# Performance work log

Measured on AMD Instinct MI355X. Metric: run time of the kernel, lower is better.

Reference implementation:

```python
import jax, jax.numpy as jnp
import numpy as np

B, H, W, C, NH = 4, 64, 64, 512, 16
HD = C // NH
BIAS_LEVEL = 0.1
LN_EPS = 1e-5


def layernorm(x, g, b):
    m = jnp.mean(x, axis=-1, keepdims=True)
    v = jnp.mean(jnp.square(x - m), axis=-1, keepdims=True)
    return (x - m) * jax.lax.rsqrt(v + LN_EPS) * g + b


def partition(x, idx):
    # x: [B, L, C] -> windows [nW, S, C]
    xg = x.reshape(B, H, W, C)
    if idx == 0:  # horizontal strips: window = one row of length W
        return xg.reshape(B * H, W, C)
    else:  # vertical strips: window = one column of length H, ordered by column
        return xg.transpose(0, 2, 1, 3).reshape(B * W, H, C)


def unpartition(w, idx):
    # w: [nW, S, C] -> [B, L, C]
    if idx == 0:
        return w.reshape(B, H * W, C)
    else:
        return w.reshape(B, W, H, C).transpose(0, 2, 1, 3).reshape(B, H * W, C)


def eg_attention(q, k, v, res_x, rpe, idx):
    # q,k,v: [B, L, C]; res_x: [B, L, C]; rpe: [1, NH, S, S]
    S = rpe.shape[-1]
    nW = (B * H * W) // S

    def to_heads(t):
        return partition(t, idx).reshape(nW, S, NH, HD).transpose(0, 2, 1, 3)

    qh, kh, vh = to_heads(q), to_heads(k), to_heads(v)  # [nW, NH, S, HD]
    attn = jnp.einsum('whsd,whtd->whst', qh, kh) + BIAS_LEVEL * rpe
    # gating mask from raw scores
    M = jnp.mean(jnp.abs(attn), axis=(1, 2, 3), keepdims=True)  # [nW,1,1,1]
    M = M / jnp.max(M)
    M = jnp.maximum(M, 0.5)
    # L2-normalize rows, trig transform
    norm = jnp.sqrt(jnp.sum(jnp.square(attn), axis=-1, keepdims=True))
    attn = attn / jnp.maximum(norm, 1e-12)
    attn = 1.0 - jnp.cos(attn * (jnp.pi / 2))
    attn = attn * M
    out = jnp.einsum('whst,whtd->whsd', attn, vh)  # [nW, NH, S, HD]
    out = out.transpose(0, 2, 1, 3).reshape(nW, S, C)
    out = unpartition(out, idx)  # [B, L, C]
    # masked residual: res_x is chunked sequentially (row-major), as in the source
    res = res_x.reshape(nW, S, C) * (1.0 - M[:, 0])
    res = res.reshape(B, H * W, C)
    return out + res


def eg_block(x, rpe, idx, ln1_g, ln1_b, wqkv, wproj, bproj, ln2_g, ln2_b,
             wfc1, bfc1, wfc2, bfc2):
    img = layernorm(x, ln1_g, ln1_b)
    qkv = img @ wqkv  # [B, L, 3C]
    q, k, v = jnp.split(qkv, 3, axis=-1)
    att = eg_attention(q, k, v, x, rpe, idx)
    att = att @ wproj + bproj
    x = x + att
    h = layernorm(x, ln2_g, ln2_b)
    h = jax.nn.gelu(h @ wfc1 + bfc1, approximate=False) @ wfc2 + bfc2
    return x + h


def setup_inputs() -> dict:
    key = jax.random.key(0)
    ks = jax.random.split(key, 16)
    d = {
        'x': jax.random.normal(ks[0], (B, H * W, C), jnp.float32),
        'rpe0': jax.random.normal(ks[1], (1, NH, W, W), jnp.float32),
        'rpe1': jax.random.normal(ks[2], (1, NH, H, H), jnp.float32),
    }
    for i, blk in enumerate(['0', '1']):
        kk = jax.random.split(ks[3 + i], 8)
        d['ln1_g' + blk] = jnp.ones((C,), jnp.float32)
        d['ln1_b' + blk] = jnp.zeros((C,), jnp.float32)
        d['wqkv' + blk] = jax.random.normal(kk[0], (C, 3 * C), jnp.float32) * 0.02
        d['wproj' + blk] = jax.random.normal(kk[1], (C, C), jnp.float32) * 0.02
        d['bproj' + blk] = jnp.zeros((C,), jnp.float32)
        d['ln2_g' + blk] = jnp.ones((C,), jnp.float32)
        d['ln2_b' + blk] = jnp.zeros((C,), jnp.float32)
        d['wfc1_' + blk] = jax.random.normal(kk[2], (C, 4 * C), jnp.float32) * 0.02
        d['bfc1_' + blk] = jnp.zeros((4 * C,), jnp.float32)
        d['wfc2_' + blk] = jax.random.normal(kk[3], (4 * C, C), jnp.float32) * 0.02
        d['bfc2_' + blk] = jnp.zeros((C,), jnp.float32)
    return d


def reference(x, rpe0, rpe1,
              ln1_g0, ln1_b0, wqkv0, wproj0, bproj0, ln2_g0, ln2_b0,
              wfc1_0, bfc1_0, wfc2_0, bfc2_0,
              ln1_g1, ln1_b1, wqkv1, wproj1, bproj1, ln2_g1, ln2_b1,
              wfc1_1, bfc1_1, wfc2_1, bfc2_1):
    x = eg_block(x, rpe0, 0, ln1_g0, ln1_b0, wqkv0, wproj0, bproj0,
                 ln2_g0, ln2_b0, wfc1_0, bfc1_0, wfc2_0, bfc2_0)
    x = eg_block(x, rpe1, 1, ln1_g1, ln1_b1, wqkv1, wproj1, bproj1,
                 ln2_g1, ln2_b1, wfc1_1, bfc1_1, wfc2_1, bfc2_1)
    return x
```

## Files before the change

### kernel.cpp

```cpp
#include <hip/hip_runtime.h>
#include <cstdint>
#include <cstddef>

typedef __bf16 bf16;
typedef __attribute__((ext_vector_type(4))) float f32x4;
typedef __attribute__((ext_vector_type(8))) __bf16 bf16x8;
typedef __attribute__((ext_vector_type(4))) __bf16 bf16x4;

static __device__ __forceinline__ f32x4 mfma16(bf16x8 a, bf16x8 b, f32x4 c) {
    return __builtin_amdgcn_mfma_f32_16x16x32_bf16(a, b, c, 0, 0, 0);
}

#define GLOAD_LDS16(gsrc, ldst)                                              \
    __builtin_amdgcn_global_load_lds(                                        \
        (const __attribute__((address_space(1))) void*)(gsrc),               \
        (__attribute__((address_space(3))) void*)(ldst), 16, 0, 0)

__global__ __launch_bounds__(256)
void transpose_cast(const float* __restrict__ W, bf16* __restrict__ Wt, int K, int N) {
    __shared__ float tile[32][33];
    const int n0 = blockIdx.x * 32, k0 = blockIdx.y * 32;
    const int tx = threadIdx.x & 31, ty = threadIdx.x >> 5;
    #pragma unroll
    for (int i = ty; i < 32; i += 8)
        tile[i][tx] = W[(size_t)(k0 + i) * N + n0 + tx];
    __syncthreads();
    #pragma unroll
    for (int i = ty; i < 32; i += 8)
        Wt[(size_t)(n0 + i) * K + k0 + tx] = (bf16)tile[tx][i];
}

__global__ __launch_bounds__(256)
void ln_kernel(const float* __restrict__ x, const float* __restrict__ g,
               const float* __restrict__ b, bf16* __restrict__ out) {
    const int row = blockIdx.x * 4 + (threadIdx.x >> 6);
    const int lane = threadIdx.x & 63;
    const float* p = x + (size_t)row * 512 + lane * 8;
    const float4 a0 = *(const float4*)p;
    const float4 a1 = *(const float4*)(p + 4);
    float vx[8] = {a0.x, a0.y, a0.z, a0.w, a1.x, a1.y, a1.z, a1.w};
    float s = 0.f, ss = 0.f;
    #pragma unroll
    for (int k = 0; k < 8; ++k) { s += vx[k]; ss += vx[k] * vx[k]; }
    #pragma unroll
    for (int m = 1; m < 64; m <<= 1) {
        s  += __shfl_xor(s, m);
        ss += __shfl_xor(ss, m);
    }
    const float mean = s * (1.0f / 512.0f);
    const float var  = ss * (1.0f / 512.0f) - mean * mean;
    const float inv  = rsqrtf(var + 1e-5f);
    const int c0 = lane * 8;
    const float4 g0 = *(const float4*)&g[c0], g1 = *(const float4*)&g[c0 + 4];
    const float4 b0 = *(const float4*)&b[c0], b1 = *(const float4*)&b[c0 + 4];
    const float gv[8] = {g0.x, g0.y, g0.z, g0.w, g1.x, g1.y, g1.z, g1.w};
    const float bv[8] = {b0.x, b0.y, b0.z, b0.w, b1.x, b1.y, b1.z, b1.w};
    bf16x8 o;
    #pragma unroll
    for (int k = 0; k < 8; ++k)
        o[k] = (bf16)((vx[k] - mean) * inv * gv[k] + bv[k]);
    *(bf16x8*)&out[(size_t)row * 512 + c0] = o;
}

template <int EPI>
__global__ __launch_bounds__(256)
void gemm_bt(const bf16* __restrict__ A, const bf16* __restrict__ Bt,
             int N, int K, const float* __restrict__ bias,
             const float* __restrict__ res, float* __restrict__ outf,
             bf16* __restrict__ outh) {
    __shared__ __align__(16) bf16 smem[16384];
    auto lsA = [&](int buf) { return smem + buf * 4096; };
    auto lsB = [&](int buf) { return smem + 8192 + buf * 4096; };
    const int nx = gridDim.x;
    const int nwg = nx * gridDim.y;
    const int flat = blockIdx.y * nx + blockIdx.x;
    const int cpx = nwg >> 3;
    const int bswz = (flat & 7) * cpx + (flat >> 3);
    const int bn = bswz % nx, bm = bswz / nx;

    const int tid = threadIdx.x, lane = tid & 63, wv = tid >> 6;
    const int wm = (wv & 1) * 64, wn = (wv >> 1) * 64;
    const int l15 = lane & 15, lg = lane >> 4;
    const size_t abase = (size_t)bm * 128 * K;
    const size_t bbase = (size_t)bn * 128 * K;
    const int srow = lane >> 2;
    const int slot = lane & 3;
    const int r0 = (wv * 2 + 0) * 16 + srow;
    const int r1 = (wv * 2 + 1) * 16 + srow;
    const int ks0 = (slot ^ ((r0 >> 1) & 3)) * 8;
    const int ks1 = (slot ^ ((r1 >> 1) & 3)) * 8;

    f32x4 acc[4][4] = {};

    auto stage = [&](int buf, int kt) {
        GLOAD_LDS16(&A[abase + (size_t)r0 * K + kt + ks0],
                    lsA(buf) + (wv * 2 + 0) * 512);
        GLOAD_LDS16(&A[abase + (size_t)r1 * K + kt + ks1],
                    lsA(buf) + (wv * 2 + 1) * 512);
        GLOAD_LDS16(&Bt[bbase + (size_t)r0 * K + kt + ks0],
                    lsB(buf) + (wv * 2 + 0) * 512);
        GLOAD_LDS16(&Bt[bbase + (size_t)r1 * K + kt + ks1],
                    lsB(buf) + (wv * 2 + 1) * 512);
    };
    auto compute = [&](int buf) {
        bf16x8 af[4], bfr[4];
        #pragma unroll
        for (int i = 0; i < 4; ++i) {
            const int r = wm + i * 16 + l15;
            af[i] = *(const bf16x8*)
                (lsA(buf) + r * 32 + ((lg ^ ((r >> 1) & 3)) * 8));
        }
        #pragma unroll
        for (int j = 0; j < 4; ++j) {
            const int r = wn + j * 16 + l15;
            bfr[j] = *(const bf16x8*)
                (lsB(buf) + r * 32 + ((lg ^ ((r >> 1) & 3)) * 8));
        }
        #pragma unroll
        for (int i = 0; i < 4; ++i)
            #pragma unroll
            for (int j = 0; j < 4; ++j)
                acc[i][j] = mfma16(af[i], bfr[j], acc[i][j]);
    };

    const int NK = K >> 5;
    stage(0, 0);
    __syncthreads();
    int cur = 0;
    for (int t = 0; t < NK - 1; ++t) {
        stage(cur ^ 1, (t + 1) * 32);
        compute(cur);
        __syncthreads();
        cur ^= 1;
    }
    compute(cur);
    __syncthreads();

    float* lsW = (float*)smem + wv * 2048;
    const int orow = bm * 128 + wm;
    const int ocol = bn * 128 + wn;
    #pragma unroll
    for (int i = 0; i < 4; ++i) {
        #pragma unroll
        for (int r = 0; r < 4; ++r)
            #pragma unroll
            for (int j = 0; j < 4; ++j)
                lsW[(lg * 4 + r) * 66 + j * 16 + l15] = acc[i][j][r];
        __builtin_amdgcn_s_waitcnt(0);
        if constexpr (EPI == 0 || EPI == 2) {
            const int rl8 = lane >> 3, c8 = (lane & 7) * 8;
            #pragma unroll
            for (int ii = 0; ii < 2; ++ii) {
                const int rl = ii * 8 + rl8;
                const float4 v0 = *(const float4*)&lsW[rl * 66 + c8];
                const float4 v1 = *(const float4*)&lsW[rl * 66 + c8 + 4];
                float vv[8] = {v0.x, v0.y, v0.z, v0.w, v1.x, v1.y, v1.z, v1.w};
                if constexpr (EPI == 2) {
                    const float4 bb0 = *(const float4*)&bias[ocol + c8];
                    const float4 bb1 = *(const float4*)&bias[ocol + c8 + 4];
                    const float bv[8] = {bb0.x, bb0.y, bb0.z, bb0.w,
                                         bb1.x, bb1.y, bb1.z, bb1.w};
                    #pragma unroll
                    for (int e = 0; e < 8; ++e) {
                        const float t = vv[e] + bv[e];
                        vv[e] = 0.5f * t * (1.0f + erff(t * 0.70710678118f));
                    }
                }
                bf16x8 o;
                #pragma unroll
                for (int e = 0; e < 8; ++e) o[e] = (bf16)vv[e];
                *(bf16x8*)&outh[(size_t)(orow + i * 16 + rl) * N + ocol + c8] = o;
            }
        } else {
            const int c4 = l15 * 4;
            const float4 bb = *(const float4*)&bias[ocol + c4];
            #pragma unroll
            for (int ii = 0; ii < 4; ++ii) {
                const int rl = ii * 4 + lg;
                const size_t gro = (size_t)(orow + i * 16 + rl) * N + ocol + c4;
                float4 v = *(const float4*)&lsW[rl * 66 + c4];
                const float4 rr = *(const float4*)&res[gro];
                v.x += bb.x + rr.x; v.y += bb.y + rr.y;
                v.z += bb.z + rr.z; v.w += bb.w + rr.w;
                *(float4*)&outf[gro] = v;
            }
        }
        __syncthreads();
    }
}

__global__ __launch_bounds__(256)
void attn_stats(const bf16* __restrict__ qkv, const float* __restrict__ rpe,
                float* __restrict__ Mraw4, int idx) {
    __shared__ float lsum[4];
    const int bid = blockIdx.x;
    const int w = bid >> 2;
    const int tid = threadIdx.x, lane = tid & 63, wv = tid >> 6;
    const int h = (bid & 3) * 4 + wv;
    const int l15 = lane & 15, lg = lane >> 4;
    const long gbase = (idx == 0) ? (long)w * 64 : ((long)(w >> 6) * 4096 + (w & 63));
    const long gstride = (idx == 0) ? 1 : 64;
    bf16x8 kf[4];
    #pragma unroll
    for (int i = 0; i < 4; ++i) {
        const long gs = gbase + (long)(i * 16 + l15) * gstride;
        kf[i] = *(const bf16x8*)&qkv[gs * 1536 + 512 + h * 32 + lg * 8];
    }
    const float* rh = rpe + h * 4096;
    float asum = 0.f;
    #pragma unroll
    for (int mi = 0; mi < 4; ++mi) {
        const long gs = gbase + (long)(mi * 16 + l15) * gstride;
        const bf16x8 qf = *(const bf16x8*)&qkv[gs * 1536 + h * 32 + lg * 8];
        f32x4 sc[4] = {};
        #pragma unroll
        for (int ni = 0; ni < 4; ++ni) sc[ni] = mfma16(qf, kf[ni], sc[ni]);
        #pragma unroll
        for (int r = 0; r < 4; ++r) {
            const int srow = mi * 16 + lg * 4 + r;
            #pragma unroll
            for (int ni = 0; ni < 4; ++ni)
                asum += fabsf(sc[ni][r] + 0.1f * rh[srow * 64 + ni * 16 + l15]);
        }
    }
    #pragma unroll
    for (int m = 1; m < 64; m <<= 1) asum += __shfl_xor(asum, m);
    if (lane == 0) lsum[wv] = asum;
    __syncthreads();
    if (tid == 0) Mraw4[bid] = lsum[0] + lsum[1] + lsum[2] + lsum[3];
}

__global__ __launch_bounds__(256)
void mcalc(const float* __restrict__ Mraw4, float* __restrict__ Mv) {
    __shared__ float red[4];
    const int t = threadIdx.x, lane = t & 63;
    const float v = (Mraw4[t * 4] + Mraw4[t * 4 + 1] + Mraw4[t * 4 + 2] +
                     Mraw4[t * 4 + 3]) * (1.0f / 65536.0f);
    float m = v;
    #pragma unroll
    for (int msk = 1; msk < 64; msk <<= 1) m = fmaxf(m, __shfl_xor(m, msk));
    if (lane == 0) red[t >> 6] = m;
    __syncthreads();
    const float mm = fmaxf(fmaxf(red[0], red[1]), fmaxf(red[2], red[3]));
    Mv[t] = fmaxf(v / mm, 0.5f);
}

__global__ __launch_bounds__(256)
void attn_apply(const bf16* __restrict__ qkv, const float* __restrict__ rpe,
                const float* __restrict__ Mv, const float* __restrict__ xin,
                bf16* __restrict__ attout, int idx) {
    __shared__ __align__(16) bf16 lsP[4][64 * 64];
    __shared__ __align__(16) bf16 lsVt[4][32 * 64];
    const int bid = blockIdx.x;
    const int w = bid >> 2;
    const int tid = threadIdx.x, lane = tid & 63, wv = tid >> 6;
    const int h = (bid & 3) * 4 + wv;
    const int l15 = lane & 15, lg = lane >> 4;
    const long gbase = (idx == 0) ? (long)w * 64 : ((long)(w >> 6) * 4096 + (w & 63));
    const long gstride = (idx == 0) ? 1 : 64;
    const float Mw = Mv[w];
    bf16* P  = lsP[wv];
    bf16* Vt = lsVt[wv];

    {
        const int d4 = (lane & 7) * 4;
        #pragma unroll
        for (int it = 0; it < 8; ++it) {
            const int t = it * 8 + (lane >> 3);
            const bf16x4 v = *(const bf16x4*)
                &qkv[(gbase + (long)t * gstride) * 1536 + 1024 + h * 32 + d4];
            #pragma unroll
            for (int e = 0; e < 4; ++e) {
                const int d = d4 + e;
                Vt[d * 64 + (t ^ ((d & 7) * 8))] = v[e];
            }
        }
    }
    bf16x8 kf[4];
    #pragma unroll
    for (int i = 0; i < 4; ++i) {
        const long gs = gbase + (long)(i * 16 + l15) * gstride;
        kf[i] = *(const bf16x8*)&qkv[gs * 1536 + 512 + h * 32 + lg * 8];
    }
    const float* rh = rpe + h * 4096;
    #pragma unroll
    for (int mi = 0; mi < 4; ++mi) {
        const long gs = gbase + (long)(mi * 16 + l15) * gstride;
        const bf16x8 qf = *(const bf16x8*)&qkv[gs * 1536 + h * 32 + lg * 8];
        f32x4 sc[4] = {};
        #pragma unroll
        for (int ni = 0; ni < 4; ++ni) sc[ni] = mfma16(qf, kf[ni], sc[ni]);
        #pragma unroll
        for (int r = 0; r < 4; ++r) {
            const int srow = mi * 16 + lg * 4 + r;
            float vv[4], ssq = 0.f;
            #pragma unroll
            for (int ni = 0; ni < 4; ++ni) {
                const float v = sc[ni][r] + 0.1f * rh[srow * 64 + ni * 16 + l15];
                vv[ni] = v;
                ssq += v * v;
            }
            ssq += __shfl_xor(ssq, 1);
            ssq += __shfl_xor(ssq, 2);
            ssq += __shfl_xor(ssq, 4);
            ssq += __shfl_xor(ssq, 8);
            const float is = 1.0f / fmaxf(sqrtf(ssq), 1e-12f);
            #pragma unroll
            for (int ni = 0; ni < 4; ++ni) {
                const float v = (1.0f - __cosf(vv[ni] * is * 1.57079632679f)) * Mw;
                const int col = ni * 16 + l15;
                P[srow * 64 + (col ^ ((srow & 7) * 8))] = (bf16)v;
            }
        }
    }
    f32x4 acc[4][2] = {};
    #pragma unroll
    for (int kk = 0; kk < 2; ++kk) {
        bf16x8 bfr[2];
        #pragma unroll
        for (int dj = 0; dj < 2; ++dj) {
            const int d = dj * 16 + l15;
            bfr[dj] = *(const bf16x8*)&Vt[d * 64 + ((kk * 32 + lg * 8) ^ ((d & 7) * 8))];
        }
        #pragma unroll
        for (int mi = 0; mi < 4; ++mi) {
            const int s = mi * 16 + l15;
            const bf16x8 af = *(const bf16x8*)&P[s * 64 + ((kk * 32 + lg * 8) ^ ((s & 7) * 8))];
            #pragma unroll
            for (int dj = 0; dj < 2; ++dj)
                acc[mi][dj] = mfma16(af, bfr[dj], acc[mi][dj]);
        }
    }
    #pragma unroll
    for (int mi = 0; mi < 4; ++mi) {
        #pragma unroll
        for (int r = 0; r < 4; ++r) {
            const int s = mi * 16 + lg * 4 + r;
            const long gg = gbase + (long)s * gstride;
            const float rm = 1.0f - Mv[(int)(gg >> 6)];
            #pragma unroll
            for (int dj = 0; dj < 2; ++dj) {
                const int d = dj * 16 + l15;
                const size_t oidx = (size_t)gg * 512 + h * 32 + d;
                attout[oidx] = (bf16)(acc[mi][dj][r] + xin[oidx] * rm);
            }
        }
    }
}

extern "C" void kernel_launch(void* const* d_in, const int* in_sizes, int n_in,
                              void* d_out, int out_size, void* d_ws, size_t ws_size,
                              hipStream_t stream) {
    const float* x    = (const float*)d_in[0];
    const float* rpe0 = (const float*)d_in[1];
    const float* rpe1 = (const float*)d_in[2];
    auto W = [&](int i) { return (const float*)d_in[i]; };

    char* ws = (char*)d_ws;
    size_t off = 0;
    auto alloc = [&](size_t bytes) {
        void* p = ws + off;
        off += (bytes + 255) & ~(size_t)255;
        return p;
    };
    bf16 *wqkvT[2], *wprojT[2], *wfc1T[2], *wfc2T[2];
    for (int b = 0; b < 2; ++b) {
        wqkvT[b] = (bf16*)alloc((size_t)1536 * 512 * 2);
        wprojT[b] = (bf16*)alloc((size_t)512 * 512 * 2);
        wfc1T[b] = (bf16*)alloc((size_t)2048 * 512 * 2);
        wfc2T[b] = (bf16*)alloc((size_t)512 * 2048 * 2);
    }
    bf16* IMG = (bf16*)alloc((size_t)16384 * 512 * 2);
    bf16* QKV = (bf16*)alloc((size_t)16384 * 1536 * 2);
    bf16* ATT = (bf16*)alloc((size_t)16384 * 512 * 2);
    bf16* H1  = QKV;
    float* X1    = (float*)alloc((size_t)16384 * 512 * 4);
    float* Mraw4 = (float*)alloc(1024 * 4);
    float* Mv    = (float*)alloc(256 * 4);
    float* XMID  = (float*)d_out;

    auto launchT = [&](const float* Wp, bf16* Wt, int K, int N) {
        transpose_cast<<<dim3(N / 32, K / 32), 256, 0, stream>>>(Wp, Wt, K, N);
    };
    launchT(W(5), wqkvT[0], 512, 1536);
    launchT(W(6), wprojT[0], 512, 512);
    launchT(W(10), wfc1T[0], 512, 2048);
    launchT(W(12), wfc2T[0], 2048, 512);
    launchT(W(16), wqkvT[1], 512, 1536);
    launchT(W(17), wprojT[1], 512, 512);
    launchT(W(21), wfc1T[1], 512, 2048);
    launchT(W(23), wfc2T[1], 2048, 512);

    for (int b = 0; b < 2; ++b) {
        const float* xin = (b == 0) ? x : X1;
        const float* rpe = (b == 0) ? rpe0 : rpe1;
        const int base = (b == 0) ? 3 : 14;
        const float* ln1g = W(base + 0);
        const float* ln1b = W(base + 1);
        const float* bproj = W(base + 4);
        const float* ln2g = W(base + 5);
        const float* ln2b = W(base + 6);
        const float* bfc1 = W(base + 8);
        const float* bfc2 = W(base + 10);

        ln_kernel<<<4096, 256, 0, stream>>>(xin, ln1g, ln1b, IMG);
        gemm_bt<0><<<dim3(12, 128), 256, 0, stream>>>(
            IMG, wqkvT[b], 1536, 512, nullptr, nullptr, nullptr, QKV);
        attn_stats<<<1024, 256, 0, stream>>>(QKV, rpe, Mraw4, b);
        mcalc<<<1, 256, 0, stream>>>(Mraw4, Mv);
        attn_apply<<<1024, 256, 0, stream>>>(QKV, rpe, Mv, xin, ATT, b);
        gemm_bt<1><<<dim3(4, 128), 256, 0, stream>>>(
            ATT, wprojT[b], 512, 512, bproj, xin, XMID, nullptr);
        ln_kernel<<<4096, 256, 0, stream>>>(XMID, ln2g, ln2b, IMG);
        gemm_bt<2><<<dim3(16, 128), 256, 0, stream>>>(
            IMG, wfc1T[b], 2048, 512, bfc1, nullptr, nullptr, H1);
        gemm_bt<1><<<dim3(4, 128), 256, 0, stream>>>(
            H1, wfc2T[b], 512, 2048, bfc2, XMID, (b == 0) ? X1 : XMID, nullptr);
    }
    (void)in_sizes; (void)n_in; (void)out_size; (void)ws_size;
}
```

Measured before the change: 479.3 us.

## Split GEMM tile across eight waves and drop per-row epilogue barrier

The bf16 GEMM now runs 512 threads per block. Each of the eight waves computes a 64x32 sub-tile of the same 128x128 block tile instead of 64x64, and each wave stages one 16-row chunk of A and B. Every wave writes its epilogue into its own smaller LDS scratch area, which allows the block-wide barrier inside the epilogue loop to be removed. The aim is more waves in flight to hide memory and MFMA latency, and fewer accumulator registers per thread. The cost is that A and B fragments are re-read from LDS more often, and the aggressive launch-bounds occupancy hint may cap registers tightly enough to cause spills.

```diff
diff --git a/kernel.cpp b/kernel.cpp
--- a/kernel.cpp
+++ b/kernel.cpp
@@ -63,7 +63,7 @@
 }
 
 template <int EPI>
-__global__ __launch_bounds__(256)
+__global__ __launch_bounds__(512, 8)
 void gemm_bt(const bf16* __restrict__ A, const bf16* __restrict__ Bt,
              int N, int K, const float* __restrict__ bias,
              const float* __restrict__ res, float* __restrict__ outf,
@@ -79,47 +79,37 @@
     const int bn = bswz % nx, bm = bswz / nx;
 
     const int tid = threadIdx.x, lane = tid & 63, wv = tid >> 6;
-    const int wm = (wv & 1) * 64, wn = (wv >> 1) * 64;
+    const int wr = wv >> 2, wc = wv & 3;
     const int l15 = lane & 15, lg = lane >> 4;
     const size_t abase = (size_t)bm * 128 * K;
     const size_t bbase = (size_t)bn * 128 * K;
-    const int srow = lane >> 2;
-    const int slot = lane & 3;
-    const int r0 = (wv * 2 + 0) * 16 + srow;
-    const int r1 = (wv * 2 + 1) * 16 + srow;
-    const int ks0 = (slot ^ ((r0 >> 1) & 3)) * 8;
-    const int ks1 = (slot ^ ((r1 >> 1) & 3)) * 8;
-
-    f32x4 acc[4][4] = {};
+    const int sr = wv * 16 + (lane >> 2);
+    const int ks = ((lane & 3) ^ ((sr >> 1) & 3)) * 8;
+
+    f32x4 acc[4][2] = {};
 
     auto stage = [&](int buf, int kt) {
-        GLOAD_LDS16(&A[abase + (size_t)r0 * K + kt + ks0],
-                    lsA(buf) + (wv * 2 + 0) * 512);
-        GLOAD_LDS16(&A[abase + (size_t)r1 * K + kt + ks1],
-                    lsA(buf) + (wv * 2 + 1) * 512);
-        GLOAD_LDS16(&Bt[bbase + (size_t)r0 * K + kt + ks0],
-                    lsB(buf) + (wv * 2 + 0) * 512);
-        GLOAD_LDS16(&Bt[bbase + (size_t)r1 * K + kt + ks1],
-                    lsB(buf) + (wv * 2 + 1) * 512);
+        GLOAD_LDS16(&A[abase + (size_t)sr * K + kt + ks], lsA(buf) + wv * 512);
+        GLOAD_LDS16(&Bt[bbase + (size_t)sr * K + kt + ks], lsB(buf) + wv * 512);
     };
     auto compute = [&](int buf) {
-        bf16x8 af[4], bfr[4];
+        bf16x8 af[4], bfr[2];
         #pragma unroll
         for (int i = 0; i < 4; ++i) {
-            const int r = wm + i * 16 + l15;
+            const int r = wr * 64 + i * 16 + l15;
             af[i] = *(const bf16x8*)
                 (lsA(buf) + r * 32 + ((lg ^ ((r >> 1) & 3)) * 8));
         }
         #pragma unroll
-        for (int j = 0; j < 4; ++j) {
-            const int r = wn + j * 16 + l15;
+        for (int j = 0; j < 2; ++j) {
+            const int r = wc * 32 + j * 16 + l15;
             bfr[j] = *(const bf16x8*)
                 (lsB(buf) + r * 32 + ((lg ^ ((r >> 1) & 3)) * 8));
         }
         #pragma unroll
         for (int i = 0; i < 4; ++i)
             #pragma unroll
-            for (int j = 0; j < 4; ++j)
+            for (int j = 0; j < 2; ++j)
                 acc[i][j] = mfma16(af[i], bfr[j], acc[i][j]);
     };
 
@@ -136,56 +126,51 @@
     compute(cur);
     __syncthreads();
 
-    float* lsW = (float*)smem + wv * 2048;
-    const int orow = bm * 128 + wm;
-    const int ocol = bn * 128 + wn;
+    float* lsW = (float*)smem + wv * 1024;
+    const int orow = bm * 128 + wr * 64;
+    const int ocol = bn * 128 + wc * 32;
     #pragma unroll
     for (int i = 0; i < 4; ++i) {
         #pragma unroll
         for (int r = 0; r < 4; ++r)
             #pragma unroll
-            for (int j = 0; j < 4; ++j)
-                lsW[(lg * 4 + r) * 66 + j * 16 + l15] = acc[i][j][r];
+            for (int j = 0; j < 2; ++j)
+                lsW[(lg * 4 + r) * 36 + j * 16 + l15] = acc[i][j][r];
         __builtin_amdgcn_s_waitcnt(0);
         if constexpr (EPI == 0 || EPI == 2) {
-            const int rl8 = lane >> 3, c8 = (lane & 7) * 8;
+            const int rl = lane >> 2, c8 = (lane & 3) * 8;
+            const float4 v0 = *(const float4*)&lsW[rl * 36 + c8];
+            const float4 v1 = *(const float4*)&lsW[rl * 36 + c8 + 4];
+            float vv[8] = {v0.x, v0.y, v0.z, v0.w, v1.x, v1.y, v1.z, v1.w};
+            if constexpr (EPI == 2) {
+                const float4 bb0 = *(const float4*)&bias[ocol + c8];
+                const float4 bb1 = *(const float4*)&bias[ocol + c8 + 4];
+                const float bv[8] = {bb0.x, bb0.y, bb0.z, bb0.w,
+                                     bb1.x, bb1.y, bb1.z, bb1.w};
+                #pragma unroll
+                for (int e = 0; e < 8; ++e) {
+                    const float t = vv[e] + bv[e];
+                    vv[e] = 0.5f * t * (1.0f + erff(t * 0.70710678118f));
+                }
+            }
+            bf16x8 o;
+            #pragma unroll
+            for (int e = 0; e < 8; ++e) o[e] = (bf16)vv[e];
+            *(bf16x8*)&outh[(size_t)(orow + i * 16 + rl) * N + ocol + c8] = o;
+        } else {
+            const int c4 = (lane & 7) * 4;
+            const float4 bb = *(const float4*)&bias[ocol + c4];
             #pragma unroll
             for (int ii = 0; ii < 2; ++ii) {
-                const int rl = ii * 8 + rl8;
-                const float4 v0 = *(const float4*)&lsW[rl * 66 + c8];
-                const float4 v1 = *(const float4*)&lsW[rl * 66 + c8 + 4];
-                float vv[8] = {v0.x, v0.y, v0.z, v0.w, v1.x, v1.y, v1.z, v1.w};
-                if constexpr (EPI == 2) {
-                    const float4 bb0 = *(const float4*)&bias[ocol + c8];
-                    const float4 bb1 = *(const float4*)&bias[ocol + c8 + 4];
-                    const float bv[8] = {bb0.x, bb0.y, bb0.z, bb0.w,
-                                         bb1.x, bb1.y, bb1.z, bb1.w};
-                    #pragma unroll
-                    for (int e = 0; e < 8; ++e) {
-                        const float t = vv[e] + bv[e];
-                        vv[e] = 0.5f * t * (1.0f + erff(t * 0.70710678118f));
-                    }
-                }
-                bf16x8 o;
-                #pragma unroll
-                for (int e = 0; e < 8; ++e) o[e] = (bf16)vv[e];
-                *(bf16x8*)&outh[(size_t)(orow + i * 16 + rl) * N + ocol + c8] = o;
-            }
-        } else {
-            const int c4 = l15 * 4;
-            const float4 bb = *(const float4*)&bias[ocol + c4];
-            #pragma unroll
-            for (int ii = 0; ii < 4; ++ii) {
-                const int rl = ii * 4 + lg;
+                const int rl = ii * 8 + (lane >> 3);
                 const size_t gro = (size_t)(orow + i * 16 + rl) * N + ocol + c4;
-                float4 v = *(const float4*)&lsW[rl * 66 + c4];
+                float4 v = *(const float4*)&lsW[rl * 36 + c4];
                 const float4 rr = *(const float4*)&res[gro];
                 v.x += bb.x + rr.x; v.y += bb.y + rr.y;
                 v.z += bb.z + rr.z; v.w += bb.w + rr.w;
                 *(float4*)&outf[gro] = v;
             }
         }
-        __syncthreads();
     }
 }
 
@@ -404,17 +389,17 @@
         const float* bfc2 = W(base + 10);
 
         ln_kernel<<<4096, 256, 0, stream>>>(xin, ln1g, ln1b, IMG);
-        gemm_bt<0><<<dim3(12, 128), 256, 0, stream>>>(
+        gemm_bt<0><<<dim3(12, 128), 512, 0, stream>>>(
             IMG, wqkvT[b], 1536, 512, nullptr, nullptr, nullptr, QKV);
         attn_stats<<<1024, 256, 0, stream>>>(QKV, rpe, Mraw4, b);
         mcalc<<<1, 256, 0, stream>>>(Mraw4, Mv);
         attn_apply<<<1024, 256, 0, stream>>>(QKV, rpe, Mv, xin, ATT, b);
-        gemm_bt<1><<<dim3(4, 128), 256, 0, stream>>>(
+        gemm_bt<1><<<dim3(4, 128), 512, 0, stream>>>(
             ATT, wprojT[b], 512, 512, bproj, xin, XMID, nullptr);
         ln_kernel<<<4096, 256, 0, stream>>>(XMID, ln2g, ln2b, IMG);
-        gemm_bt<2><<<dim3(16, 128), 256, 0, stream>>>(
+        gemm_bt<2><<<dim3(16, 128), 512, 0, stream>>>(
             IMG, wfc1T[b], 2048, 512, bfc1, nullptr, nullptr, H1);
-        gemm_bt<1><<<dim3(4, 128), 256, 0, stream>>>(
+        gemm_bt<1><<<dim3(4, 128), 512, 0, stream>>>(
             H1, wfc2T[b], 512, 2048, bfc2, XMID, (b == 0) ? X1 : XMID, nullptr);
     }
     (void)in_sizes; (void)n_in; (void)out_size; (void)ws_size;
```

Result: faster. 462.9 us (-3.4%).
